# Optimization experiments

Hardware: AMD Instinct MI355X
Metric: run time of the kernel (lower is better)

The kernel has to match this reference:

```python
import jax, jax.numpy as jnp
import numpy as np

B, T, DIM, H = 4, 2048, 1024, 16
NOPE, ROPE, VDIM, KVR = 128, 64, 128, 512
QKD = NOPE + ROPE  # 192
SCALE = QKD ** -0.5
THETA = 10000.0


def apply_rope(x, cos, sin):
    # x: (B, T, H, D) with interleaved (real, imag) pairs; cos/sin: (T, D//2)
    xr, xi = x[..., 0::2], x[..., 1::2]
    c = cos[None, :, None, :]
    s = sin[None, :, None, :]
    yr = xr * c - xi * s
    yi = xr * s + xi * c
    return jnp.stack([yr, yi], axis=-1).reshape(x.shape)


def rms_norm(x, eps=1e-6):
    return x * jax.lax.rsqrt(jnp.mean(x * x, axis=-1, keepdims=True) + eps)


def setup_inputs() -> dict:
    key = jax.random.key(0)
    ks = jax.random.split(key, 10)
    def lin(k, fan_in, fan_out):
        bound = 1.0 / np.sqrt(fan_in)
        kw, kb = jax.random.split(k)
        w = jax.random.uniform(kw, (fan_out, fan_in), jnp.float32, -bound, bound)
        b = jax.random.uniform(kb, (fan_out,), jnp.float32, -bound, bound)
        return w, b
    wq_w, wq_b = lin(ks[0], DIM, H * QKD)
    wkv_a_w, wkv_a_b = lin(ks[1], DIM, KVR + ROPE)
    wkv_b_w, wkv_b_b = lin(ks[2], KVR, H * (NOPE + VDIM))
    wo_w, wo_b = lin(ks[3], H * VDIM, DIM)
    x = jax.random.normal(ks[4], (B, T, DIM), jnp.float32)
    inv_freq = THETA ** (-jnp.arange(0, ROPE, 2, dtype=jnp.float32) / ROPE)  # (32,)
    ang = jnp.arange(T, dtype=jnp.float32)[:, None] * inv_freq[None, :]  # (T, 32)
    return {
        "x": x,
        "wq_w": wq_w, "wq_b": wq_b,
        "wkv_a_w": wkv_a_w, "wkv_a_b": wkv_a_b,
        "wkv_b_w": wkv_b_w, "wkv_b_b": wkv_b_b,
        "wo_w": wo_w, "wo_b": wo_b,
        "freqs_cos": jnp.cos(ang), "freqs_sin": jnp.sin(ang),
        "start_pos": 0,
    }


def reference(x, wq_w, wq_b, wkv_a_w, wkv_a_b, wkv_b_w, wkv_b_b, wo_w, wo_b,
              freqs_cos, freqs_sin, start_pos):
    b, t, _ = x.shape
    # Q projection, split into nope + rope parts
    q = (x @ wq_w.T + wq_b).reshape(b, t, H, QKD)
    q_nope, q_rope = q[..., :NOPE], q[..., NOPE:]
    q_rope = apply_rope(q_rope, freqs_cos, freqs_sin)
    q = jnp.concatenate([q_nope, q_rope], axis=-1)  # (B,T,H,192)
    # low-rank KV latent + shared rope key
    kv_a = x @ wkv_a_w.T + wkv_a_b  # (B,T,576)
    kv_lat, k_rope = kv_a[..., :KVR], kv_a[..., KVR:]
    k_rope = apply_rope(k_rope[:, :, None, :], freqs_cos, freqs_sin)  # (B,T,1,64)
    # decompress latent -> k_nope, v
    kv = (rms_norm(kv_lat) @ wkv_b_w.T + wkv_b_b).reshape(b, t, H, NOPE + VDIM)
    k_nope, v = kv[..., :NOPE], kv[..., NOPE:]
    k = jnp.concatenate([k_nope, jnp.broadcast_to(k_rope, (b, t, H, ROPE))], axis=-1)
    # causal SDPA (start_pos=0 prefill: cache[:end_pos] == current k/v)
    scores = jnp.einsum("bthd,bshd->bhts", q, k) * SCALE
    causal = jnp.tril(jnp.ones((t, t), dtype=bool))
    scores = jnp.where(causal[None, None], scores, jnp.finfo(scores.dtype).min)
    probs = jax.nn.softmax(scores, axis=-1)
    out = jnp.einsum("bhts,bshd->bthd", probs, v).reshape(b, t, H * VDIM)
    return out @ wo_w.T + wo_b
```

## Files before the change

kernel.cpp:

```cpp
#include <hip/hip_runtime.h>
#include <hip/hip_bf16.h>
#include <cmath>

#define B_    4
#define T_    2048
#define DIM_  1024
#define H_    16
#define NOPE_ 128
#define ROPE_ 64
#define VDIM_ 128
#define KVR_  512
#define QKD_  192
#define NTOK  (B_ * T_)

static constexpr float SCALE2_ = 0.07216878364870322f * 1.4426950408889634f;

typedef __attribute__((ext_vector_type(8))) unsigned short ushort8_t;
typedef __bf16 v8bf __attribute__((ext_vector_type(8)));
typedef float  v4f  __attribute__((ext_vector_type(4)));
typedef unsigned int v4u __attribute__((ext_vector_type(4)));

__device__ __forceinline__ float bf2f(unsigned short u) {
    return __uint_as_float(((unsigned int)u) << 16);
}
__device__ __forceinline__ unsigned short f2bf(float f) {
    unsigned int u = __float_as_uint(f);
    u += 0x7FFFu + ((u >> 16) & 1u);
    return (unsigned short)(u >> 16);
}
__device__ __forceinline__ unsigned short f2bf_hw(float f) {
    return __builtin_bit_cast(unsigned short, (__bf16)f);
}
__device__ __forceinline__ unsigned int cvt_pk_bf16(float lo, float hi) {
    unsigned int r;
    asm("v_cvt_pk_bf16_f32 %0, %1, %2" : "=v"(r) : "v"(lo), "v"(hi));
    return r;
}
__device__ __forceinline__ void store1(float* p, float v)          { *p = v; }
__device__ __forceinline__ void store1(__hip_bfloat16* p, float v) { *p = __float2bfloat16(v); }

__device__ __forceinline__ float exp2_hw(float x) {
    return __builtin_amdgcn_exp2f(x);
}

__device__ __forceinline__ void load_lds16(const void* g, void* l) {
    __builtin_amdgcn_global_load_lds(
        (const __attribute__((address_space(1))) void*)g,
        (__attribute__((address_space(3))) void*)l, 16, 0, 0);
}

__device__ __forceinline__ void cvt4(const float* s, __hip_bfloat16* d, int q4) {
    const int i = q4 * 4;
    const float4 v = *(const float4*)(s + i);
    ushort4 o;
    o.x = f2bf(v.x); o.y = f2bf(v.y); o.z = f2bf(v.z); o.w = f2bf(v.w);
    *(ushort4*)((unsigned short*)d + i) = o;
}

#define X4_   (NTOK*1024/4)
#define Q4_   (3072*1024/4)
#define KB4_  (4096*512/4)
#define O4_   (1024*2048/4)
#define A4_   (640*1024/4)
#define CVT_TOTAL (X4_ + Q4_ + KB4_ + O4_ + A4_)

__global__ __launch_bounds__(256) void cvt_all(
    const float* __restrict__ x,    const float* __restrict__ wq,
    const float* __restrict__ wkvb, const float* __restrict__ wo,
    const float* __restrict__ wkva, const float* __restrict__ wkva_bias,
    __hip_bfloat16* __restrict__ xb,    __hip_bfloat16* __restrict__ wqb,
    __hip_bfloat16* __restrict__ wkvbb, __hip_bfloat16* __restrict__ wob,
    __hip_bfloat16* __restrict__ wkvab, float* __restrict__ bias_pad)
{
    int idx = blockIdx.x * 256 + threadIdx.x;
    if (idx < X4_) { cvt4(x, xb, idx); return; }
    idx -= X4_;
    if (idx < Q4_) { cvt4(wq, wqb, idx); return; }
    idx -= Q4_;
    if (idx < KB4_) { cvt4(wkvb, wkvbb, idx); return; }
    idx -= KB4_;
    if (idx < O4_) { cvt4(wo, wob, idx); return; }
    idx -= O4_;
    if (idx < A4_) {
        const int i = idx * 4;
        ushort4 o;
        if (i < 576 * 1024) {
            const float4 v = *(const float4*)(wkva + i);
            o.x = f2bf(v.x); o.y = f2bf(v.y); o.z = f2bf(v.z); o.w = f2bf(v.w);
        } else {
            o.x = o.y = o.z = o.w = 0;
        }
        *(ushort4*)((unsigned short*)wkvab + i) = o;
        if (idx < 640) bias_pad[idx] = (idx < 576) ? wkva_bias[idx] : 0.0f;
    }
}

template <typename CT, int EPI>
__global__ __launch_bounds__(256) void gemm_mfma(
    const __hip_bfloat16* __restrict__ A, int lda,
    const __hip_bfloat16* __restrict__ W, int ldw,
    const float* __restrict__ bias,
    CT* __restrict__ C, int ldc, int K,
    unsigned short* __restrict__ kvf)
{
    __shared__ unsigned short smem[2 * 128 * 32];
    unsigned short* A_s = smem;
    unsigned short* B_s = smem + 128 * 32;

    const int tid  = threadIdx.x;
    const int ln   = tid & 63;
    const int wv   = tid >> 6;
    const int l15  = ln & 15;
    const int quad = ln >> 4;
    const int wm   = wv & 1, wn = wv >> 1;

    const int nwx = (int)gridDim.x, nwy = (int)gridDim.y;
    const int flat = (int)blockIdx.x + nwx * (int)blockIdx.y;
    const int cpx = (nwx * nwy) >> 3;
    const int swz = (flat & 7) * cpx + (flat >> 3);
    const int n0 = (swz / nwy) * 128, m0 = (swz % nwy) * 128;

    v4f acc[4][4] = {};

    for (int k0 = 0; k0 < K; k0 += 32) {
        __syncthreads();
        #pragma unroll
        for (int it = 0; it < 2; ++it) {
            const int idx = it * 256 + wv * 64;
            const int li  = idx + ln;
            const int row = li >> 2, ch = li & 3;
            load_lds16(A + (size_t)(m0 + row) * lda + k0 + ch * 8, &A_s[idx * 8]);
            load_lds16(W + (size_t)(n0 + row) * ldw + k0 + ch * 8, &B_s[idx * 8]);
        }
        __syncthreads();

        v8bf af[4], bf_[4];
        #pragma unroll
        for (int i = 0; i < 4; ++i) {
            af[i]  = *(const v8bf*)&A_s[(wm * 64 + i * 16 + l15) * 32 + quad * 8];
            bf_[i] = *(const v8bf*)&B_s[(wn * 64 + i * 16 + l15) * 32 + quad * 8];
        }
        #pragma unroll
        for (int i = 0; i < 4; ++i)
            #pragma unroll
            for (int j = 0; j < 4; ++j)
                acc[i][j] = __builtin_amdgcn_mfma_f32_16x16x32_bf16(
                                af[i], bf_[j], acc[i][j], 0, 0, 0);
    }

    if (EPI == 0) {
        #pragma unroll
        for (int i = 0; i < 4; ++i) {
            const int mrow = m0 + wm * 64 + i * 16 + quad * 4;
            #pragma unroll
            for (int j = 0; j < 4; ++j) {
                const int ncol = n0 + wn * 64 + j * 16 + l15;
                const float bb = bias[ncol];
                #pragma unroll
                for (int r = 0; r < 4; ++r)
                    store1(C + (size_t)(mrow + r) * ldc + ncol, acc[i][j][r] + bb);
            }
        }
    } else {
        const int head = n0 >> 8;
        const bool is_v = (n0 & 128) != 0;
        __syncthreads();
        #pragma unroll
        for (int p = 0; p < 2; ++p) {
            if (p) __syncthreads();
            if (wm == p) {
                #pragma unroll
                for (int i = 0; i < 4; ++i) {
                    #pragma unroll
                    for (int j = 0; j < 4; ++j) {
                        const int ncl = wn * 64 + j * 16 + l15;
                        const float bb = bias[n0 + ncl];
                        #pragma unroll
                        for (int r = 0; r < 4; ++r) {
                            const unsigned short v = f2bf(acc[i][j][r] + bb);
                            const int lnf = quad * 4 + r;
                            int off;
                            if (!is_v) {
                                const int s = ncl >> 5, qf = (ncl >> 3) & 3, e = ncl & 7;
                                off = (s * 4 + i) * 512 + (qf * 16 + lnf) * 8 + e;
                            } else {
                                const int nt = ncl >> 4, lnv = ncl & 15;
                                const int jj = i * 16 + lnf;
                                const int s2 = jj >> 5, qv = (jj >> 3) & 3, ev = jj & 7;
                                off = (nt * 2 + s2) * 512 + (qv * 16 + lnv) * 8 + ev;
                            }
                            smem[off] = v;
                        }
                    }
                }
            }
            __syncthreads();
            const size_t GT = (size_t)(m0 >> 6) + p;
            unsigned short* dst = kvf + ((GT * 16 + head) << 14) + (is_v ? 16 * 512 : 0);
            #pragma unroll
            for (int it = 0; it < 4; ++it) {
                const int u = (tid + it * 256) * 8;
                *(ushort8_t*)(dst + u) = *(const ushort8_t*)&smem[u];
            }
        }
    }
}

__global__ __launch_bounds__(256) void gemm_qkva(
    const __hip_bfloat16* __restrict__ A,
    const __hip_bfloat16* __restrict__ Wq, const float* __restrict__ biasq,
    __hip_bfloat16* __restrict__ Cq,
    const __hip_bfloat16* __restrict__ Wa, const float* __restrict__ biasa,
    __hip_bfloat16* __restrict__ Ca)
{
    __shared__ unsigned short smem[2 * 128 * 32];
    unsigned short* A_s = smem;
    unsigned short* B_s = smem + 128 * 32;

    const int flat = (int)blockIdx.x + 29 * (int)blockIdx.y;
    const int swz  = (flat & 7) * (1856 >> 3) + (flat >> 3);
    const int xw   = swz / 64, yw = swz % 64;

    const bool is_q = xw < 24;
    const __hip_bfloat16* W = is_q ? Wq : Wa;
    const float* bias       = is_q ? biasq : biasa;
    __hip_bfloat16* C       = is_q ? Cq : Ca;
    const int ldc = is_q ? 3072 : 640;
    const int n0  = (is_q ? xw : (xw - 24)) * 128;
    const int m0  = yw * 128;

    const int tid  = threadIdx.x;
    const int ln   = tid & 63;
    const int wv   = tid >> 6;
    const int l15  = ln & 15;
    const int quad = ln >> 4;
    const int wm   = wv & 1, wn = wv >> 1;

    v4f acc[4][4] = {};

    for (int k0 = 0; k0 < 1024; k0 += 32) {
        __syncthreads();
        #pragma unroll
        for (int it = 0; it < 2; ++it) {
            const int idx = it * 256 + wv * 64;
            const int li  = idx + ln;
            const int row = li >> 2, ch = li & 3;
            load_lds16(A + (size_t)(m0 + row) * 1024 + k0 + ch * 8, &A_s[idx * 8]);
            load_lds16(W + (size_t)(n0 + row) * 1024 + k0 + ch * 8, &B_s[idx * 8]);
        }
        __syncthreads();

        v8bf af[4], bf_[4];
        #pragma unroll
        for (int i = 0; i < 4; ++i) {
            af[i]  = *(const v8bf*)&A_s[(wm * 64 + i * 16 + l15) * 32 + quad * 8];
            bf_[i] = *(const v8bf*)&B_s[(wn * 64 + i * 16 + l15) * 32 + quad * 8];
        }
        #pragma unroll
        for (int i = 0; i < 4; ++i)
            #pragma unroll
            for (int j = 0; j < 4; ++j)
                acc[i][j] = __builtin_amdgcn_mfma_f32_16x16x32_bf16(
                                af[i], bf_[j], acc[i][j], 0, 0, 0);
    }

    #pragma unroll
    for (int i = 0; i < 4; ++i) {
        const int mrow = m0 + wm * 64 + i * 16 + quad * 4;
        #pragma unroll
        for (int j = 0; j < 4; ++j) {
            const int ncol = n0 + wn * 64 + j * 16 + l15;
            const float bb = bias[ncol];
            #pragma unroll
            for (int r = 0; r < 4; ++r)
                C[(size_t)(mrow + r) * ldc + ncol] = __float2bfloat16(acc[i][j][r] + bb);
        }
    }
}

__global__ __launch_bounds__(256) void rmsnorm_ropek(
    const __hip_bfloat16* __restrict__ kva,
    __hip_bfloat16* __restrict__ kvn,
    __hip_bfloat16* __restrict__ kr,
    const float* __restrict__ cs,
    const float* __restrict__ sn)
{
    const int tok = blockIdx.x;
    const int tid = threadIdx.x;
    const __hip_bfloat16* row = kva + (size_t)tok * 640;

    const float x0 = __bfloat162float(row[tid]);
    const float x1 = __bfloat162float(row[tid + 256]);
    float ss = x0*x0 + x1*x1;
    #pragma unroll
    for (int off = 32; off >= 1; off >>= 1)
        ss += __shfl_down(ss, off);

    __shared__ float red[4];
    __shared__ float scale_sh;
    if ((tid & 63) == 0) red[tid >> 6] = ss;
    __syncthreads();
    if (tid == 0) {
        const float tot = red[0] + red[1] + red[2] + red[3];
        scale_sh = rsqrtf(tot * (1.0f/512.0f) + 1e-6f);
    }
    __syncthreads();
    const float sc = scale_sh;
    kvn[(size_t)tok*512 + tid]       = __float2bfloat16(x0 * sc);
    kvn[(size_t)tok*512 + tid + 256] = __float2bfloat16(x1 * sc);

    if (tid < 32) {
        const int t = tok & (T_ - 1);
        const float c = cs[t*32 + tid];
        const float s = sn[t*32 + tid];
        const float xr = __bfloat162float(row[KVR_ + 2*tid]);
        const float xi = __bfloat162float(row[KVR_ + 2*tid + 1]);
        kr[(size_t)tok*64 + 2*tid]     = __float2bfloat16(xr * c - xi * s);
        kr[(size_t)tok*64 + 2*tid + 1] = __float2bfloat16(xr * s + xi * c);
    }
}

__device__ __forceinline__ void attn_stage_regs(
    v8bf* R,
    const unsigned short* __restrict__ kvf,
    const __hip_bfloat16* __restrict__ kr,
    size_t tokb, int j0, int h, int wv, int lane, int tid)
{
    const size_t GT = (tokb + j0) >> 6;
    const unsigned short* base = kvf + ((GT * 16 + h) << 14);
    #pragma unroll
    for (int i = 0; i < 4; ++i)
        R[i] = *(const v8bf*)(base + ((wv * 4 + i) << 9) + lane * 8);
    const int j = tid >> 3, dch = tid & 7;
    R[4] = *(const v8bf*)((const unsigned short*)kr + (tokb + j0 + j) * 64 + dch * 8);
}

__global__ __launch_bounds__(512, 2) void attn_mfma(
    const __hip_bfloat16* __restrict__ q,
    const unsigned short* __restrict__ kvf,
    const __hip_bfloat16* __restrict__ kr,
    const float* __restrict__ cs,
    const float* __restrict__ sn,
    __hip_bfloat16* __restrict__ att)
{
    __shared__ unsigned short KVf[2][40 * 512];

    const int tid  = threadIdx.x;
    const int lane = tid & 63;
    const int ln   = tid & 15;
    const int quad = (tid >> 4) & 3;
    const int wv   = tid >> 6;
    const int hf   = quad >> 1;
    const int p2   = quad & 1;

    const int bid  = (int)(blockIdx.x + 8u * blockIdx.y + 128u * blockIdx.z);
    const int half = bid >> 8;
    const int id2  = bid & 255;
    const int pr   = id2 & 3;
    const int h    = (id2 >> 2) & 15;
    const int b    = id2 >> 6;
    const int qt   = half ? pr : (7 - pr);

    const int q0 = qt * 256;
    const size_t tokb = (size_t)b * T_;

    v8bf qf[2][6];
    #pragma unroll
    for (int st = 0; st < 2; ++st) {
        const int trow = q0 + st*128 + wv*16 + ln;
        const __hip_bfloat16* qrow =
            q + (tokb + trow) * (size_t)(H_*QKD_) + h*QKD_;
        #pragma unroll
        for (int s = 0; s < 6; ++s) {
            ushort8_t raw = *(const ushort8_t*)(qrow + s*32 + quad*8);
            ushort8_t o;
            if (s < 4) {
                #pragma unroll
                for (int i = 0; i < 8; ++i)
                    o[i] = f2bf_hw(bf2f(raw[i]) * SCALE2_);
            } else {
                #pragma unroll
                for (int pp2 = 0; pp2 < 4; ++pp2) {
                    const int fi = (s-4)*16 + quad*4 + pp2;
                    const float c  = cs[trow*32 + fi];
                    const float sv = sn[trow*32 + fi];
                    const float xr = bf2f(raw[pp2*2]);
                    const float xi = bf2f(raw[pp2*2+1]);
                    o[pp2*2]   = f2bf_hw((xr*c - xi*sv) * SCALE2_);
                    o[pp2*2+1] = f2bf_hw((xr*sv + xi*c) * SCALE2_);
                }
            }
            qf[st][s] = __builtin_bit_cast(v8bf, o);
        }
    }

    v4f O[2][8];
    #pragma unroll
    for (int st = 0; st < 2; ++st)
        #pragma unroll
        for (int nt = 0; nt < 8; ++nt) O[st][nt] = (v4f){0.f, 0.f, 0.f, 0.f};
    float m_r[2] = {-1e30f, -1e30f};
    float l_r[2] = {0.0f, 0.0f};

    const int qmin0 = q0 + wv*16;
    const int qmin1 = q0 + 128 + wv*16;
    const int nkt = (q0 + 256) >> 6;

    const int slot0 = (wv < 4) ? (wv * 4) : (wv * 4 + 8);
    const int krj = tid >> 3, krd = tid & 7;
    const int krfrag = 16 + (krd >> 2) * 4 + (krj >> 4);
    const int kroff  = krfrag * 512 + ((krd & 3) * 16 + (krj & 15)) * 8;

    v8bf R[5];
    attn_stage_regs(R, kvf, kr, tokb, 0, h, wv, lane, tid);
    {
        unsigned short* Kw = KVf[0];
        #pragma unroll
        for (int i = 0; i < 4; ++i)
            *(v8bf*)&Kw[(slot0 + i) * 512 + lane * 8] = R[i];
        *(v8bf*)&Kw[kroff] = R[4];
    }

    for (int kt = 0; kt < nkt; ++kt) {
        const int j0 = kt << 6;
        const int cur = kt & 1;
        const unsigned short* Kb = KVf[cur];

        __syncthreads();

        if (kt + 1 < nkt)
            attn_stage_regs(R, kvf, kr, tokb, j0 + 64, h, wv, lane, tid);

        const bool act0 = (j0 <= qmin0 + 15);
        const bool act1 = (j0 <= qmin1 + 15);

        if (act1) {
            v4f S[2][4];
            #pragma unroll
            for (int st = 0; st < 2; ++st)
                #pragma unroll
                for (int t = 0; t < 4; ++t) S[st][t] = (v4f){0.f, 0.f, 0.f, 0.f};
            __builtin_amdgcn_s_setprio(1);
            if (act0) {
                #pragma unroll
                for (int s = 0; s < 6; ++s)
                    #pragma unroll
                    for (int t = 0; t < 4; ++t) {
                        const v8bf kb = *(const v8bf*)&Kb[(s*4 + t)*512 + lane*8];
                        S[0][t] = __builtin_amdgcn_mfma_f32_16x16x32_bf16(kb, qf[0][s], S[0][t], 0, 0, 0);
                        S[1][t] = __builtin_amdgcn_mfma_f32_16x16x32_bf16(kb, qf[1][s], S[1][t], 0, 0, 0);
                    }
            } else {
                #pragma unroll
                for (int s = 0; s < 6; ++s)
                    #pragma unroll
                    for (int t = 0; t < 4; ++t) {
                        const v8bf kb = *(const v8bf*)&Kb[(s*4 + t)*512 + lane*8];
                        S[1][t] = __builtin_amdgcn_mfma_f32_16x16x32_bf16(kb, qf[1][s], S[1][t], 0, 0, 0);
                    }
            }
            __builtin_amdgcn_s_setprio(0);

            v8bf pfrag[2][2];
            #pragma unroll
            for (int st = 0; st < 2; ++st) {
                if (st == 0 && !act0) continue;
                const int qmin = (st == 0) ? qmin0 : qmin1;
                const int qrow = qmin + ln;
                if (j0 + 63 > qmin) {
                    #pragma unroll
                    for (int t = 0; t < 4; ++t) {
                        const int kbase = j0 + t*16 + quad*4;
                        #pragma unroll
                        for (int r = 0; r < 4; ++r)
                            if (kbase + r > qrow) S[st][t][r] = -1e30f;
                    }
                }
                float mx = S[st][0][0];
                #pragma unroll
                for (int t = 0; t < 4; ++t)
                    #pragma unroll
                    for (int r = 0; r < 4; ++r)
                        if (t || r) mx = fmaxf(mx, S[st][t][r]);
                mx = fmaxf(mx, __shfl_xor(mx, 16));
                mx = fmaxf(mx, __shfl_xor(mx, 32));
                const bool need = mx > m_r[st] + 8.0f;
                if (__any((int)need)) {
                    const float mn = fmaxf(m_r[st], mx);
                    const float alpha = exp2_hw(m_r[st] - mn);
                    m_r[st] = mn;
                    l_r[st] *= alpha;
                    #pragma unroll
                    for (int nt = 0; nt < 8; ++nt)
                        O[st][nt] *= alpha;
                }
                float rs = 0.0f;
                #pragma unroll
                for (int t = 0; t < 4; ++t)
                    #pragma unroll
                    for (int r = 0; r < 4; ++r) {
                        const float pp = exp2_hw(S[st][t][r] - m_r[st]);
                        S[st][t][r] = pp;
                        rs += pp;
                    }
                rs += __shfl_xor(rs, 16);
                rs += __shfl_xor(rs, 32);
                l_r[st] += rs;
                unsigned int pk[4][2];
                #pragma unroll
                for (int t = 0; t < 4; ++t)
                    #pragma unroll
                    for (int i = 0; i < 2; ++i)
                        pk[t][i] = cvt_pk_bf16(S[st][t][2*i], S[st][t][2*i+1]);
                #pragma unroll
                for (int s2 = 0; s2 < 2; ++s2) {
                    const unsigned int A0 = pk[2*s2][0],   A1 = pk[2*s2][1];
                    const unsigned int B0 = pk[2*s2+1][0], B1 = pk[2*s2+1][1];
                    const unsigned int sB0 = __shfl_xor(B0, 32), sB1 = __shfl_xor(B1, 32);
                    const unsigned int sA0 = __shfl_xor(A0, 32), sA1 = __shfl_xor(A1, 32);
                    const unsigned int U0 = hf ? sB0 : A0;
                    const unsigned int U1 = hf ? sB1 : A1;
                    const unsigned int V0 = hf ? B0 : sA0;
                    const unsigned int V1 = hf ? B1 : sA1;
                    const unsigned int xU0 = __shfl_xor(U0, 16), xU1 = __shfl_xor(U1, 16);
                    const unsigned int xV0 = __shfl_xor(V0, 16), xV1 = __shfl_xor(V1, 16);
                    v4u w;
                    w.x = p2 ? xV0 : U0;
                    w.y = p2 ? xV1 : U1;
                    w.z = p2 ? V0 : xU0;
                    w.w = p2 ? V1 : xU1;
                    pfrag[st][s2] = __builtin_bit_cast(v8bf, w);
                }
            }

            __builtin_amdgcn_s_setprio(1);
            #pragma unroll
            for (int s2 = 0; s2 < 2; ++s2) {
                if (act0) {
                    #pragma unroll
                    for (int nt = 0; nt < 8; ++nt) {
                        const v8bf vb = *(const v8bf*)&Kb[(24 + nt*2 + s2)*512 + lane*8];
                        O[0][nt] = __builtin_amdgcn_mfma_f32_16x16x32_bf16(vb, pfrag[0][s2], O[0][nt], 0, 0, 0);
                        O[1][nt] = __builtin_amdgcn_mfma_f32_16x16x32_bf16(vb, pfrag[1][s2], O[1][nt], 0, 0, 0);
                    }
                } else {
                    #pragma unroll
                    for (int nt = 0; nt < 8; ++nt) {
                        const v8bf vb = *(const v8bf*)&Kb[(24 + nt*2 + s2)*512 + lane*8];
                        O[1][nt] = __builtin_amdgcn_mfma_f32_16x16x32_bf16(vb, pfrag[1][s2], O[1][nt], 0, 0, 0);
                    }
                }
            }
            __builtin_amdgcn_s_setprio(0);
        }

        if (kt + 1 < nkt) {
            unsigned short* Kw = KVf[cur ^ 1];
            #pragma unroll
            for (int i = 0; i < 4; ++i)
                *(v8bf*)&Kw[(slot0 + i) * 512 + lane * 8] = R[i];
            *(v8bf*)&Kw[kroff] = R[4];
        }
    }

    #pragma unroll
    for (int st = 0; st < 2; ++st) {
        const int qrow = q0 + st*128 + wv*16 + ln;
        const float inv = 1.0f / l_r[st];
        unsigned short* orow =
            (unsigned short*)att + (tokb + qrow) * (size_t)(H_*VDIM_) + h*VDIM_;
        #pragma unroll
        for (int nt = 0; nt < 8; ++nt) {
            #pragma unroll
            for (int rp = 0; rp < 2; ++rp) {
                const unsigned int w =
                    cvt_pk_bf16(O[st][nt][2*rp] * inv, O[st][nt][2*rp+1] * inv);
                *(unsigned int*)(orow + nt*16 + quad*4 + rp*2) = w;
            }
        }
    }
}

__global__ void fill_zero(float* p, int n) {
    int i = blockIdx.x * 256 + threadIdx.x;
    if (i < n) p[i] = 0.0f;
}

extern "C" void kernel_launch(void* const* d_in, const int* in_sizes, int n_in,
                              void* d_out, int out_size, void* d_ws, size_t ws_size,
                              hipStream_t stream)
{
    const float* x      = (const float*)d_in[0];
    const float* wq_w   = (const float*)d_in[1];
    const float* wq_b   = (const float*)d_in[2];
    const float* wkva_w = (const float*)d_in[3];
    const float* wkva_b = (const float*)d_in[4];
    const float* wkvb_w = (const float*)d_in[5];
    const float* wkvb_b = (const float*)d_in[6];
    const float* wo_w   = (const float*)d_in[7];
    const float* wo_b   = (const float*)d_in[8];
    const float* cs     = (const float*)d_in[9];
    const float* sn     = (const float*)d_in[10];

    const size_t q_b    = (size_t)NTOK * 3072 * 2;
    const size_t kvf_b  = (size_t)128 * 16 * 32 * 512 * 2;
    const size_t xb_b   = (size_t)NTOK * 1024 * 2;
    const size_t kvap_b = (size_t)NTOK * 640 * 2;
    const size_t kvn_b  = (size_t)NTOK * 512 * 2;
    const size_t wq_b_b = (size_t)3072 * 1024 * 2;
    const size_t wkva_b_b = (size_t)640 * 1024 * 2;
    const size_t wkvb_b_b = (size_t)4096 * 512 * 2;
    const size_t wo_b_b   = (size_t)1024 * 2048 * 2;
    const size_t bias_b   = 4096;
    const size_t need = q_b + kvf_b + xb_b + kvap_b + kvn_b +
                        wq_b_b + wkva_b_b + wkvb_b_b + wo_b_b + bias_b;

    if (ws_size < need) {
        fill_zero<<<(out_size + 255) / 256, 256, 0, stream>>>((float*)d_out, out_size);
        return;
    }

    char* p = (char*)d_ws;
    __hip_bfloat16* q    = (__hip_bfloat16*)p;             p += q_b;
    unsigned short* kvf  = (unsigned short*)p;             p += kvf_b;
    char*           dynr = p;
    __hip_bfloat16* xb   = (__hip_bfloat16*)p;             p += xb_b;
    __hip_bfloat16* kvap = (__hip_bfloat16*)p;             p += kvap_b;
    __hip_bfloat16* kvn  = (__hip_bfloat16*)p;             p += kvn_b;
    __hip_bfloat16* wq_bf = (__hip_bfloat16*)p;
    __hip_bfloat16* kr    = (__hip_bfloat16*)p;            p += wq_b_b;
    __hip_bfloat16* wkva_bf = (__hip_bfloat16*)p;          p += wkva_b_b;
    __hip_bfloat16* wkvb_bf = (__hip_bfloat16*)p;          p += wkvb_b_b;
    __hip_bfloat16* wo_bf   = (__hip_bfloat16*)p;          p += wo_b_b;
    float*          bias_pad = (float*)p;
    __hip_bfloat16* attb = (__hip_bfloat16*)dynr;
    float*          out  = (float*)d_out;

    cvt_all<<<CVT_TOTAL / 256, 256, 0, stream>>>(
        x, wq_w, wkvb_w, wo_w, wkva_w, wkva_b,
        xb, wq_bf, wkvb_bf, wo_bf, wkva_bf, bias_pad);

    gemm_qkva<<<dim3(29, NTOK/128), 256, 0, stream>>>(
        xb, wq_bf, wq_b, q, wkva_bf, bias_pad, kvap);

    rmsnorm_ropek<<<NTOK, 256, 0, stream>>>(kvap, kvn, kr, cs, sn);

    gemm_mfma<__hip_bfloat16, 1><<<dim3(4096/128, NTOK/128), 256, 0, stream>>>(
        kvn, 512, wkvb_bf, 512, wkvb_b, (( __hip_bfloat16*)nullptr), 0, 512, kvf);

    attn_mfma<<<dim3(T_/256, H_, B_), 512, 0, stream>>>(q, kvf, kr, cs, sn, attb);

    gemm_mfma<float, 0><<<dim3(1024/128, NTOK/128), 256, 0, stream>>>(
        attb, 2048, wo_bf, 2048, wo_b, out, 1024, 2048, nullptr);
}
```

Baseline: 480.1 us.

## Double-buffer GEMM LDS tiles and interleave per-subtile softmax with PV MFMAs

The two projection GEMM kernels now double-buffer their LDS tiles. The next K-slice is prefetched while MFMAs run on the current one, which cuts one barrier per iteration and hides load latency. In the attention kernel, softmax and the PV product now run per query subtile (subtile 1, then subtile 0) instead of doing both softmaxes before both PV passes. This lets one subtile's PV MFMAs overlap with the other subtile's softmax VALU work. The trade-off is twice the LDS per GEMM block, which may lower occupancy, and more reliance on the compiler's instruction scheduling.

```diff
diff --git a/kernel.cpp b/kernel.cpp
--- a/kernel.cpp
+++ b/kernel.cpp
@@ -1,6 +1,7 @@
 #include <hip/hip_runtime.h>
 #include <hip/hip_bf16.h>
 #include <cmath>
+#include <type_traits>
 
 #define B_    4
 #define T_    2048
@@ -19,6 +20,10 @@
 typedef __bf16 v8bf __attribute__((ext_vector_type(8)));
 typedef float  v4f  __attribute__((ext_vector_type(4)));
 typedef unsigned int v4u __attribute__((ext_vector_type(4)));
+
+template <int N> using ic = std::integral_constant<int, N>;
+
+struct PFrag { v8bf a, b; };
 
 __device__ __forceinline__ float bf2f(unsigned short u) {
     return __uint_as_float(((unsigned int)u) << 16);
@@ -95,6 +100,22 @@
     }
 }
 
+__device__ __forceinline__ void gemm_stage(
+    const __hip_bfloat16* __restrict__ A, int lda,
+    const __hip_bfloat16* __restrict__ W, int ldw,
+    int m0, int n0, int k0,
+    unsigned short* A_s, unsigned short* B_s, int wv, int ln)
+{
+    #pragma unroll
+    for (int it = 0; it < 2; ++it) {
+        const int idx = it * 256 + wv * 64;
+        const int li  = idx + ln;
+        const int row = li >> 2, ch = li & 3;
+        load_lds16(A + (size_t)(m0 + row) * lda + k0 + ch * 8, &A_s[idx * 8]);
+        load_lds16(W + (size_t)(n0 + row) * ldw + k0 + ch * 8, &B_s[idx * 8]);
+    }
+}
+
 template <typename CT, int EPI>
 __global__ __launch_bounds__(256) void gemm_mfma(
     const __hip_bfloat16* __restrict__ A, int lda,
@@ -103,9 +124,7 @@
     CT* __restrict__ C, int ldc, int K,
     unsigned short* __restrict__ kvf)
 {
-    __shared__ unsigned short smem[2 * 128 * 32];
-    unsigned short* A_s = smem;
-    unsigned short* B_s = smem + 128 * 32;
+    __shared__ unsigned short smem[2 * 8192];
 
     const int tid  = threadIdx.x;
     const int ln   = tid & 63;
@@ -122,17 +141,17 @@
 
     v4f acc[4][4] = {};
 
+    gemm_stage(A, lda, W, ldw, m0, n0, 0, smem, smem + 4096, wv, ln);
+    __syncthreads();
+
+    int cur = 0;
     for (int k0 = 0; k0 < K; k0 += 32) {
-        __syncthreads();
-        #pragma unroll
-        for (int it = 0; it < 2; ++it) {
-            const int idx = it * 256 + wv * 64;
-            const int li  = idx + ln;
-            const int row = li >> 2, ch = li & 3;
-            load_lds16(A + (size_t)(m0 + row) * lda + k0 + ch * 8, &A_s[idx * 8]);
-            load_lds16(W + (size_t)(n0 + row) * ldw + k0 + ch * 8, &B_s[idx * 8]);
-        }
-        __syncthreads();
+        if (k0 + 32 < K)
+            gemm_stage(A, lda, W, ldw, m0, n0, k0 + 32,
+                       smem + (cur ^ 1) * 8192, smem + (cur ^ 1) * 8192 + 4096,
+                       wv, ln);
+        const unsigned short* A_s = smem + cur * 8192;
+        const unsigned short* B_s = A_s + 4096;
 
         v8bf af[4], bf_[4];
         #pragma unroll
@@ -146,6 +165,8 @@
             for (int j = 0; j < 4; ++j)
                 acc[i][j] = __builtin_amdgcn_mfma_f32_16x16x32_bf16(
                                 af[i], bf_[j], acc[i][j], 0, 0, 0);
+        __syncthreads();
+        cur ^= 1;
     }
 
     if (EPI == 0) {
@@ -164,7 +185,6 @@
     } else {
         const int head = n0 >> 8;
         const bool is_v = (n0 & 128) != 0;
-        __syncthreads();
         #pragma unroll
         for (int p = 0; p < 2; ++p) {
             if (p) __syncthreads();
@@ -213,9 +233,7 @@
     const __hip_bfloat16* __restrict__ Wa, const float* __restrict__ biasa,
     __hip_bfloat16* __restrict__ Ca)
 {
-    __shared__ unsigned short smem[2 * 128 * 32];
-    unsigned short* A_s = smem;
-    unsigned short* B_s = smem + 128 * 32;
+    __shared__ unsigned short smem[2 * 8192];
 
     const int flat = (int)blockIdx.x + 29 * (int)blockIdx.y;
     const int swz  = (flat & 7) * (1856 >> 3) + (flat >> 3);
@@ -238,17 +256,17 @@
 
     v4f acc[4][4] = {};
 
+    gemm_stage(A, 1024, W, 1024, m0, n0, 0, smem, smem + 4096, wv, ln);
+    __syncthreads();
+
+    int cur = 0;
     for (int k0 = 0; k0 < 1024; k0 += 32) {
-        __syncthreads();
-        #pragma unroll
-        for (int it = 0; it < 2; ++it) {
-            const int idx = it * 256 + wv * 64;
-            const int li  = idx + ln;
-            const int row = li >> 2, ch = li & 3;
-            load_lds16(A + (size_t)(m0 + row) * 1024 + k0 + ch * 8, &A_s[idx * 8]);
-            load_lds16(W + (size_t)(n0 + row) * 1024 + k0 + ch * 8, &B_s[idx * 8]);
-        }
-        __syncthreads();
+        if (k0 + 32 < 1024)
+            gemm_stage(A, 1024, W, 1024, m0, n0, k0 + 32,
+                       smem + (cur ^ 1) * 8192, smem + (cur ^ 1) * 8192 + 4096,
+                       wv, ln);
+        const unsigned short* A_s = smem + cur * 8192;
+        const unsigned short* B_s = A_s + 4096;
 
         v8bf af[4], bf_[4];
         #pragma unroll
@@ -262,6 +280,8 @@
             for (int j = 0; j < 4; ++j)
                 acc[i][j] = __builtin_amdgcn_mfma_f32_16x16x32_bf16(
                                 af[i], bf_[j], acc[i][j], 0, 0, 0);
+        __syncthreads();
+        cur ^= 1;
     }
 
     #pragma unroll
@@ -440,32 +460,10 @@
             for (int st = 0; st < 2; ++st)
                 #pragma unroll
                 for (int t = 0; t < 4; ++t) S[st][t] = (v4f){0.f, 0.f, 0.f, 0.f};
-            __builtin_amdgcn_s_setprio(1);
-            if (act0) {
-                #pragma unroll
-                for (int s = 0; s < 6; ++s)
-                    #pragma unroll
-                    for (int t = 0; t < 4; ++t) {
-                        const v8bf kb = *(const v8bf*)&Kb[(s*4 + t)*512 + lane*8];
-                        S[0][t] = __builtin_amdgcn_mfma_f32_16x16x32_bf16(kb, qf[0][s], S[0][t], 0, 0, 0);
-                        S[1][t] = __builtin_amdgcn_mfma_f32_16x16x32_bf16(kb, qf[1][s], S[1][t], 0, 0, 0);
-                    }
-            } else {
-                #pragma unroll
-                for (int s = 0; s < 6; ++s)
-                    #pragma unroll
-                    for (int t = 0; t < 4; ++t) {
-                        const v8bf kb = *(const v8bf*)&Kb[(s*4 + t)*512 + lane*8];
-                        S[1][t] = __builtin_amdgcn_mfma_f32_16x16x32_bf16(kb, qf[1][s], S[1][t], 0, 0, 0);
-                    }
-            }
-            __builtin_amdgcn_s_setprio(0);
-
-            v8bf pfrag[2][2];
-            #pragma unroll
-            for (int st = 0; st < 2; ++st) {
-                if (st == 0 && !act0) continue;
-                const int qmin = (st == 0) ? qmin0 : qmin1;
+
+            auto SM = [&](auto STc) -> PFrag {
+                constexpr int ST = STc.value;
+                const int qmin = (ST == 0) ? qmin0 : qmin1;
                 const int qrow = qmin + ln;
                 if (j0 + 63 > qmin) {
                     #pragma unroll
@@ -473,45 +471,49 @@
                         const int kbase = j0 + t*16 + quad*4;
                         #pragma unroll
                         for (int r = 0; r < 4; ++r)
-                            if (kbase + r > qrow) S[st][t][r] = -1e30f;
+                            if (kbase + r > qrow) S[ST][t][r] = -1e30f;
                     }
                 }
-                float mx = S[st][0][0];
-                #pragma unroll
-                for (int t = 0; t < 4; ++t)
-                    #pragma unroll
-                    for (int r = 0; r < 4; ++r)
-                        if (t || r) mx = fmaxf(mx, S[st][t][r]);
+                float m0_ = fmaxf(fmaxf(S[ST][0][0], S[ST][0][1]),
+                                  fmaxf(S[ST][0][2], S[ST][0][3]));
+                float m1_ = fmaxf(fmaxf(S[ST][1][0], S[ST][1][1]),
+                                  fmaxf(S[ST][1][2], S[ST][1][3]));
+                float m2_ = fmaxf(fmaxf(S[ST][2][0], S[ST][2][1]),
+                                  fmaxf(S[ST][2][2], S[ST][2][3]));
+                float m3_ = fmaxf(fmaxf(S[ST][3][0], S[ST][3][1]),
+                                  fmaxf(S[ST][3][2], S[ST][3][3]));
+                float mx = fmaxf(fmaxf(m0_, m1_), fmaxf(m2_, m3_));
                 mx = fmaxf(mx, __shfl_xor(mx, 16));
                 mx = fmaxf(mx, __shfl_xor(mx, 32));
-                const bool need = mx > m_r[st] + 8.0f;
+                const bool need = mx > m_r[ST] + 8.0f;
                 if (__any((int)need)) {
-                    const float mn = fmaxf(m_r[st], mx);
-                    const float alpha = exp2_hw(m_r[st] - mn);
-                    m_r[st] = mn;
-                    l_r[st] *= alpha;
+                    const float mn = fmaxf(m_r[ST], mx);
+                    const float alpha = exp2_hw(m_r[ST] - mn);
+                    m_r[ST] = mn;
+                    l_r[ST] *= alpha;
                     #pragma unroll
                     for (int nt = 0; nt < 8; ++nt)
-                        O[st][nt] *= alpha;
+                        O[ST][nt] *= alpha;
                 }
                 float rs = 0.0f;
                 #pragma unroll
                 for (int t = 0; t < 4; ++t)
                     #pragma unroll
                     for (int r = 0; r < 4; ++r) {
-                        const float pp = exp2_hw(S[st][t][r] - m_r[st]);
-                        S[st][t][r] = pp;
+                        const float pp = exp2_hw(S[ST][t][r] - m_r[ST]);
+                        S[ST][t][r] = pp;
                         rs += pp;
                     }
                 rs += __shfl_xor(rs, 16);
                 rs += __shfl_xor(rs, 32);
-                l_r[st] += rs;
+                l_r[ST] += rs;
                 unsigned int pk[4][2];
                 #pragma unroll
                 for (int t = 0; t < 4; ++t)
                     #pragma unroll
                     for (int i = 0; i < 2; ++i)
-                        pk[t][i] = cvt_pk_bf16(S[st][t][2*i], S[st][t][2*i+1]);
+                        pk[t][i] = cvt_pk_bf16(S[ST][t][2*i], S[ST][t][2*i+1]);
+                PFrag out;
                 #pragma unroll
                 for (int s2 = 0; s2 < 2; ++s2) {
                     const unsigned int A0 = pk[2*s2][0],   A1 = pk[2*s2][1];
@@ -529,29 +531,58 @@
                     w.y = p2 ? xV1 : U1;
                     w.z = p2 ? V0 : xU0;
                     w.w = p2 ? V1 : xU1;
-                    pfrag[st][s2] = __builtin_bit_cast(v8bf, w);
+                    if (s2 == 0) out.a = __builtin_bit_cast(v8bf, w);
+                    else         out.b = __builtin_bit_cast(v8bf, w);
                 }
-            }
-
-            __builtin_amdgcn_s_setprio(1);
-            #pragma unroll
-            for (int s2 = 0; s2 < 2; ++s2) {
-                if (act0) {
+                return out;
+            };
+
+            auto PV = [&](auto STc, v8bf pf0, v8bf pf1) {
+                constexpr int ST = STc.value;
+                __builtin_amdgcn_s_setprio(1);
+                #pragma unroll
+                for (int s2 = 0; s2 < 2; ++s2) {
+                    const v8bf pfx = s2 ? pf1 : pf0;
                     #pragma unroll
                     for (int nt = 0; nt < 8; ++nt) {
                         const v8bf vb = *(const v8bf*)&Kb[(24 + nt*2 + s2)*512 + lane*8];
-                        O[0][nt] = __builtin_amdgcn_mfma_f32_16x16x32_bf16(vb, pfrag[0][s2], O[0][nt], 0, 0, 0);
-                        O[1][nt] = __builtin_amdgcn_mfma_f32_16x16x32_bf16(vb, pfrag[1][s2], O[1][nt], 0, 0, 0);
-                    }
-                } else {
-                    #pragma unroll
-                    for (int nt = 0; nt < 8; ++nt) {
-                        const v8bf vb = *(const v8bf*)&Kb[(24 + nt*2 + s2)*512 + lane*8];
-                        O[1][nt] = __builtin_amdgcn_mfma_f32_16x16x32_bf16(vb, pfrag[1][s2], O[1][nt], 0, 0, 0);
+                        O[ST][nt] = __builtin_amdgcn_mfma_f32_16x16x32_bf16(
+                                        vb, pfx, O[ST][nt], 0, 0, 0);
                     }
                 }
+                __builtin_amdgcn_s_setprio(0);
+            };
+
+            __builtin_amdgcn_s_setprio(1);
+            if (act0) {
+                #pragma unroll
+                for (int s = 0; s < 6; ++s)
+                    #pragma unroll
+                    for (int t = 0; t < 4; ++t) {
+                        const v8bf kb = *(const v8bf*)&Kb[(s*4 + t)*512 + lane*8];
+                        S[1][t] = __builtin_amdgcn_mfma_f32_16x16x32_bf16(kb, qf[1][s], S[1][t], 0, 0, 0);
+                        S[0][t] = __builtin_amdgcn_mfma_f32_16x16x32_bf16(kb, qf[0][s], S[0][t], 0, 0, 0);
+                    }
+            } else {
+                #pragma unroll
+                for (int s = 0; s < 6; ++s)
+                    #pragma unroll
+                    for (int t = 0; t < 4; ++t) {
+                        const v8bf kb = *(const v8bf*)&Kb[(s*4 + t)*512 + lane*8];
+                        S[1][t] = __builtin_amdgcn_mfma_f32_16x16x32_bf16(kb, qf[1][s], S[1][t], 0, 0, 0);
+                    }
             }
             __builtin_amdgcn_s_setprio(0);
+
+            if (act0) {
+                PFrag p1 = SM(ic<1>{});
+                PV(ic<1>{}, p1.a, p1.b);
+                PFrag p0 = SM(ic<0>{});
+                PV(ic<0>{}, p0.a, p0.b);
+            } else {
+                PFrag p1 = SM(ic<1>{});
+                PV(ic<1>{}, p1.a, p1.b);
+            }
         }
 
         if (kt + 1 < nkt) {
```

After: 466.2 us. 2.9% less time.
